# Performance work log

Hardware: AMD Instinct MI355X
Metric: run time of the kernel (lower is better)

The kernel has to match this reference:

```python
import jax, jax.numpy as jnp
import numpy as np

EMBED_DIM = 1024
NUM_HEADS = 16
HEAD_DIM = EMBED_DIM // NUM_HEADS
BATCH = 2
SEQ = 2048


def setup_inputs() -> dict:
    key = jax.random.key(0)
    k_x, k_wi, k_bi, k_wo, k_bo = jax.random.split(key, 5)
    scale_in = 1.0 / np.sqrt(EMBED_DIM)
    x = jax.random.normal(k_x, (BATCH, SEQ, EMBED_DIM), dtype=jnp.float32)
    # nn.Linear stores weight [out, in]; we keep [in, out] for x @ W.
    w_in = jax.random.uniform(k_wi, (EMBED_DIM, 3 * EMBED_DIM), jnp.float32, -scale_in, scale_in)
    b_in = jax.random.uniform(k_bi, (3 * EMBED_DIM,), jnp.float32, -scale_in, scale_in)
    w_out = jax.random.uniform(k_wo, (EMBED_DIM, EMBED_DIM), jnp.float32, -scale_in, scale_in)
    b_out = jax.random.uniform(k_bo, (EMBED_DIM,), jnp.float32, -scale_in, scale_in)
    return {"x": x, "w_in": w_in, "b_in": b_in, "w_out": w_out, "b_out": b_out}


def reference(x, w_in, b_in, w_out, b_out):
    B, S, E = x.shape
    H, D = NUM_HEADS, HEAD_DIM
    inp = x @ w_in + b_in                       # [B,S,3E]
    que, key, val = jnp.split(inp, 3, axis=-1)  # each [B,S,E]
    que = que.reshape(B, S, H, D)
    key = key.reshape(B, S, H, D)
    val = val.reshape(B, S, H, D)
    scores = jnp.einsum('bshd,brhd->bhsr', que, key) * (1.0 / np.sqrt(D))
    weights = jax.nn.softmax(scores, axis=-1)   # [B,H,S,S]
    attn = jnp.einsum('bhsr,brhd->bshd', weights, val).reshape(B, S, E)
    return attn @ w_out + b_out
```

## Files before the change

### kernel.cpp

```cpp
#include <hip/hip_runtime.h>


typedef __bf16 bf16x8 __attribute__((ext_vector_type(8)));
typedef float  f32x4  __attribute__((ext_vector_type(4)));
typedef short  s16x4  __attribute__((ext_vector_type(4)));
typedef short  s16x8  __attribute__((ext_vector_type(8)));

__device__ __forceinline__ unsigned short f2b(float f) {
  unsigned u = __float_as_uint(f);
  unsigned r = u + 0x7fffu + ((u >> 16) & 1u);
  return (unsigned short)(r >> 16);
}

__device__ __forceinline__ unsigned cvt_pk_bf16(float a, float b) {
#if defined(__HIP_DEVICE_COMPILE__)
  unsigned r;
  asm("v_cvt_pk_bf16_f32 %0, %1, %2" : "=v"(r) : "v"(a), "v"(b));
  return r;
#else
  return (unsigned)f2b(a) | ((unsigned)f2b(b) << 16);
#endif
}

__device__ __forceinline__ void gl_lds16(const void* g, void* l) {
  __builtin_amdgcn_global_load_lds(
      (__attribute__((address_space(1))) void*)g,
      (__attribute__((address_space(3))) void*)l, 16, 0, 0);
}

__device__ __forceinline__ f32x4 mfma16x16x16(s16x4 a, s16x4 b, f32x4 c) {
#if defined(__HIP_DEVICE_COMPILE__)
#if __has_builtin(__builtin_amdgcn_mfma_f32_16x16x16bf16_1k)
  return __builtin_amdgcn_mfma_f32_16x16x16bf16_1k(a, b, c, 0, 0, 0);
#else
  s16x8 a8 = {a[0], a[1], a[2], a[3], 0, 0, 0, 0};
  s16x8 b8 = {b[0], b[1], b[2], b[3], 0, 0, 0, 0};
  union U { s16x8 s; bf16x8 v; };
  U ua, ub; ua.s = a8; ub.s = b8;
  return __builtin_amdgcn_mfma_f32_16x16x32_bf16(ua.v, ub.v, c, 0, 0, 0);
#endif
#else
  (void)a; (void)b;
  return c;
#endif
}

__device__ __forceinline__ void transpose_cast_body(
    const float* __restrict__ in, unsigned short* __restrict__ out,
    int R, int C, int bx, int by, int tid, float tile[64][65]) {
  int r0 = by * 64, c0 = bx * 64;
#pragma unroll
  for (int p = 0; p < 16; p++) {
    int i = tid + p * 256;
    int ri = i >> 6, ci = i & 63;
    tile[ri][ci] = in[(size_t)(r0 + ri) * C + c0 + ci];
  }
  __syncthreads();
#pragma unroll
  for (int p = 0; p < 16; p++) {
    int i = tid + p * 256;
    int ci = i >> 6, ri = i & 63;
    out[(size_t)(c0 + ci) * R + r0 + ri] = f2b(tile[ri][ci]);
  }
}

__global__ __launch_bounds__(256) void prep_kernel(
    const float* __restrict__ x, unsigned short* __restrict__ xb,
    const float* __restrict__ w_in, unsigned short* __restrict__ wint,
    const float* __restrict__ w_out, unsigned short* __restrict__ woutt) {
  __shared__ float tile[64][65];
  int bid = blockIdx.x, tid = threadIdx.x;
  if (bid < 4096) {
    int i = bid * 256 + tid;
    float4 v = ((const float4*)x)[i];
    ushort4 o;
    o.x = f2b(v.x); o.y = f2b(v.y); o.z = f2b(v.z); o.w = f2b(v.w);
    ((ushort4*)xb)[i] = o;
  } else if (bid < 4864) {
    int l = bid - 4096;
    transpose_cast_body(w_in, wint, 1024, 3072, l % 48, l / 48, tid, tile);
  } else {
    int l = bid - 4864;
    transpose_cast_body(w_out, woutt, 1024, 1024, l % 16, l / 16, tid, tile);
  }
}

__global__ __launch_bounds__(256) void vt_transpose_kernel(
    const unsigned short* __restrict__ qkv, unsigned short* __restrict__ vt) {
  __shared__ unsigned short tile[64][65];
  int bid = blockIdx.x;
  int st = bid & 31, h = (bid >> 5) & 15, b = bid >> 9;
  int s0 = st * 64;
  int tid = threadIdx.x;
  const unsigned short* src = qkv + (size_t)(b * 2048 + s0) * 3072 + 2048 + h * 64;
#pragma unroll
  for (int p = 0; p < 16; p++) {
    int i = tid + p * 256;
    int sr = i >> 6, d = i & 63;
    tile[sr][d] = src[(size_t)sr * 3072 + d];
  }
  __syncthreads();
  unsigned short* dst = vt + (size_t)(b * 16 + h) * 64 * 2048 + s0;
#pragma unroll
  for (int p = 0; p < 16; p++) {
    int i = tid + p * 256;
    int dr = i >> 6, sc = i & 63;
    dst[(size_t)dr * 2048 + sc] = tile[sc][dr];
  }
}

__global__ __launch_bounds__(256) void gemm_bt1(
    const unsigned short* __restrict__ A, const unsigned short* __restrict__ Bt,
    const float* __restrict__ bias, unsigned short* __restrict__ Cp,
    int M, int N, int K, int qcols, float qscale) {
  __shared__ __align__(16) unsigned short As[128 * 32];
  __shared__ __align__(16) unsigned short Bs[128 * 32];
  int tid = threadIdx.x;
  int wave = tid >> 6, lane = tid & 63;
  int m_l = lane & 15, quad = lane >> 4;
  int wm = (wave >> 1) * 64, wn = (wave & 1) * 64;
  int row = tid >> 2, kp = (tid & 3) << 3;
  const unsigned short* ag = A + (size_t)(blockIdx.y * 128 + row) * K + kp;
  const unsigned short* bg = Bt + (size_t)(blockIdx.x * 128 + row) * K + kp;
  unsigned short* asw = As + wave * 512;
  unsigned short* bsw = Bs + wave * 512;
  f32x4 acc[4][4] = {};
  for (int k0 = 0; k0 < K; k0 += 32) {
    __syncthreads();
    gl_lds16(ag + k0, asw);
    gl_lds16(ag + (size_t)64 * K + k0, asw + 2048);
    gl_lds16(bg + k0, bsw);
    gl_lds16(bg + (size_t)64 * K + k0, bsw + 2048);
    __syncthreads();
    bf16x8 af[4], bf[4];
#pragma unroll
    for (int i = 0; i < 4; i++)
      af[i] = *(const bf16x8*)&As[(wm + i * 16 + m_l) * 32 + quad * 8];
#pragma unroll
    for (int j = 0; j < 4; j++)
      bf[j] = *(const bf16x8*)&Bs[(wn + j * 16 + m_l) * 32 + quad * 8];
#pragma unroll
    for (int i = 0; i < 4; i++)
#pragma unroll
      for (int j = 0; j < 4; j++)
        acc[i][j] = __builtin_amdgcn_mfma_f32_16x16x32_bf16(af[i], bf[j], acc[i][j], 0, 0, 0);
  }
  float bv[4];
#pragma unroll
  for (int j = 0; j < 4; j++) bv[j] = bias[blockIdx.x * 128 + wn + j * 16 + m_l];
#pragma unroll
  for (int i = 0; i < 4; i++) {
    int m = blockIdx.y * 128 + wm + i * 16 + quad * 4;
#pragma unroll
    for (int j = 0; j < 4; j++) {
      int n = blockIdx.x * 128 + wn + j * 16 + m_l;
      float sc = (n < qcols) ? qscale : 1.0f;
#pragma unroll
      for (int r = 0; r < 4; r++) {
        float v = (acc[i][j][r] + bv[j]) * sc;
        Cp[(size_t)(m + r) * N + n] = f2b(v);
      }
    }
  }
}

__global__ __launch_bounds__(256) void gemm_bt2(
    const unsigned short* __restrict__ A, const unsigned short* __restrict__ Bt,
    const float* __restrict__ bias, float* __restrict__ Cp, int M, int N, int K) {
  __shared__ __align__(16) unsigned short As[128 * 32];
  __shared__ __align__(16) unsigned short Bs[64 * 32];
  int tid = threadIdx.x;
  int wave = tid >> 6, lane = tid & 63;
  int m_l = lane & 15, quad = lane >> 4;
  int wm = (wave >> 1) * 64, wn = (wave & 1) * 32;
  int row = tid >> 2, kp = (tid & 3) << 3;
  const unsigned short* ag = A + (size_t)(blockIdx.y * 128 + row) * K + kp;
  const unsigned short* bg = Bt + (size_t)(blockIdx.x * 64 + row) * K + kp;
  unsigned short* asw = As + wave * 512;
  unsigned short* bsw = Bs + wave * 512;
  f32x4 acc[4][2] = {};
  for (int k0 = 0; k0 < K; k0 += 32) {
    __syncthreads();
    gl_lds16(ag + k0, asw);
    gl_lds16(ag + (size_t)64 * K + k0, asw + 2048);
    gl_lds16(bg + k0, bsw);
    __syncthreads();
    bf16x8 af[4], bf[2];
#pragma unroll
    for (int i = 0; i < 4; i++)
      af[i] = *(const bf16x8*)&As[(wm + i * 16 + m_l) * 32 + quad * 8];
#pragma unroll
    for (int j = 0; j < 2; j++)
      bf[j] = *(const bf16x8*)&Bs[(wn + j * 16 + m_l) * 32 + quad * 8];
#pragma unroll
    for (int i = 0; i < 4; i++)
#pragma unroll
      for (int j = 0; j < 2; j++)
        acc[i][j] = __builtin_amdgcn_mfma_f32_16x16x32_bf16(af[i], bf[j], acc[i][j], 0, 0, 0);
  }
  float bv[2];
#pragma unroll
  for (int j = 0; j < 2; j++) bv[j] = bias[blockIdx.x * 64 + wn + j * 16 + m_l];
#pragma unroll
  for (int i = 0; i < 4; i++) {
    int m = blockIdx.y * 128 + wm + i * 16 + quad * 4;
#pragma unroll
    for (int j = 0; j < 2; j++) {
      int n = blockIdx.x * 64 + wn + j * 16 + m_l;
#pragma unroll
      for (int r = 0; r < 4; r++)
        Cp[(size_t)(m + r) * N + n] = acc[i][j][r] + bv[j];
    }
  }
}

__global__ __launch_bounds__(512) void attn_kernel(
    const unsigned short* __restrict__ qkv, const unsigned short* __restrict__ vt,
    unsigned short* __restrict__ aout) {
  __shared__ __align__(16) unsigned short Qs[128 * 64];
  __shared__ __align__(16) unsigned short Ks[64 * 64];
  __shared__ __align__(16) unsigned short Vts[64 * 64];
  int bid = blockIdx.x;
  int qt = bid & 15, h = (bid >> 4) & 15, b = bid >> 8;
  int tid = threadIdx.x, wave = tid >> 6;
  int lane = tid & 63;
  int m_l = lane & 15, quad = lane >> 4;
  int q0 = qt * 128;
  const unsigned short* qb = qkv + (size_t)b * 2048 * 3072 + h * 64;
  const unsigned short* kb = qb + 1024;
  const unsigned short* vtb = vt + (size_t)(b * 16 + h) * 64 * 2048;

  int srow = tid >> 3;
  int sd0 = ((tid & 7) ^ (srow & 7)) * 8;

  gl_lds16(qb + (size_t)(q0 + srow) * 3072 + sd0, Qs + wave * 512);
  gl_lds16(qb + (size_t)(q0 + 64 + srow) * 3072 + sd0, Qs + 4096 + wave * 512);
  __syncthreads();

  int ml7 = m_l & 7;
  int sw0 = ((quad ^ ml7) * 8);
  int sw1 = (((quad + 4) ^ ml7) * 8);

  int qrow = (wave * 16 + m_l) * 64;
  bf16x8 qf0 = *(const bf16x8*)&Qs[qrow + sw0];
  bf16x8 qf1 = *(const bf16x8*)&Qs[qrow + sw1];

  int kbase = m_l * 64;
  int vbase = m_l * 64 + (quad & 1) * 4;
  int qh = quad >> 1;

  const s16x4 ones = {0x3F80, 0x3F80, 0x3F80, 0x3F80};

  f32x4 o[4] = {};
  f32x4 lacc = {};

  for (int kt = 0; kt < 2048; kt += 64) {
    __syncthreads();
    gl_lds16(kb + (size_t)(kt + srow) * 3072 + sd0, Ks + wave * 512);
    gl_lds16(vtb + (size_t)srow * 2048 + kt + sd0, Vts + wave * 512);
    __syncthreads();

#pragma unroll
    for (int t = 0; t < 4; t++) {
      bf16x8 kf0 = *(const bf16x8*)&Ks[kbase + t * 1024 + sw0];
      bf16x8 kf1 = *(const bf16x8*)&Ks[kbase + t * 1024 + sw1];
      f32x4 z = {};
      f32x4 s = __builtin_amdgcn_mfma_f32_16x16x32_bf16(kf0, qf0, z, 0, 0, 0);
      s = __builtin_amdgcn_mfma_f32_16x16x32_bf16(kf1, qf1, s, 0, 0, 0);
      union { uint2 u; s16x4 s4; } pk;
      pk.u.x = cvt_pk_bf16(__builtin_exp2f(s[0]), __builtin_exp2f(s[1]));
      pk.u.y = cvt_pk_bf16(__builtin_exp2f(s[2]), __builtin_exp2f(s[3]));
      lacc = mfma16x16x16(ones, pk.s4, lacc);
      int voff = vbase + (((t * 2 + qh) ^ ml7) * 8);
#pragma unroll
      for (int dt = 0; dt < 4; dt++) {
        s16x4 vf = *(const s16x4*)&Vts[voff + dt * 1024];
        o[dt] = mfma16x16x16(vf, pk.s4, o[dt]);
      }
    }
  }

  float rl = 1.0f / lacc[0];

  unsigned short* ob = aout + (size_t)(b * 2048 + q0 + wave * 16 + m_l) * 1024 +
                       h * 64 + quad * 4;
#pragma unroll
  for (int dt = 0; dt < 4; dt++) {
    union { uint2 u; ushort4 w; } pk;
    pk.u.x = cvt_pk_bf16(o[dt][0] * rl, o[dt][1] * rl);
    pk.u.y = cvt_pk_bf16(o[dt][2] * rl, o[dt][3] * rl);
    *(ushort4*)&ob[dt * 16] = pk.w;
  }
}

extern "C" void kernel_launch(void* const* d_in, const int* in_sizes, int n_in,
                              void* d_out, int out_size, void* d_ws, size_t ws_size,
                              hipStream_t stream) {
  (void)in_sizes; (void)n_in; (void)out_size; (void)ws_size;
  const float* x     = (const float*)d_in[0];
  const float* w_in  = (const float*)d_in[1];
  const float* b_in  = (const float*)d_in[2];
  const float* w_out = (const float*)d_in[3];
  const float* b_out = (const float*)d_in[4];
  char* ws = (char*)d_ws;
  unsigned short* xb    = (unsigned short*)(ws + 0);
  unsigned short* wint  = (unsigned short*)(ws + 8388608);
  unsigned short* woutt = (unsigned short*)(ws + 14680064);
  unsigned short* qkv   = (unsigned short*)(ws + 16777216);
  unsigned short* vt    = (unsigned short*)(ws + 41943040);
  unsigned short* attn  = (unsigned short*)(ws + 50331648);
  float* out = (float*)d_out;

  const float QSCALE = 0.125f * 1.44269504088896f;

  prep_kernel<<<5120, 256, 0, stream>>>(x, xb, w_in, wint, w_out, woutt);
  gemm_bt1<<<dim3(24, 32), 256, 0, stream>>>(xb, wint, b_in, qkv, 4096, 3072, 1024,
                                             1024, QSCALE);
  vt_transpose_kernel<<<1024, 256, 0, stream>>>(qkv, vt);
  attn_kernel<<<512, 512, 0, stream>>>(qkv, vt, attn);
  gemm_bt2<<<dim3(16, 32), 256, 0, stream>>>(attn, woutt, b_out, out, 4096, 1024, 1024);
}
```

Before: 207.6 us.

## Rewrite attention inner loop with 32x32x16 MFMA and permlane32 swaps

The attention kernel moves from 16x16 MFMA tiles with 8 waves per block to 32x32x16 MFMA tiles with 4 waves per block, each wave covering 32 query rows. The row sum is now accumulated on VALU from the exponentials instead of with an extra MFMA against a ones vector. The P fragments for the PV product are re-laid out in registers with v_permlane32_swap. The aim is fewer MFMA instructions, fewer LDS fragment reads per FLOP, and no redundant sum-MFMA, at the cost of more registers per wave and fewer waves per block.

```diff
diff --git a/kernel.cpp b/kernel.cpp
--- a/kernel.cpp
+++ b/kernel.cpp
@@ -3,6 +3,7 @@
 
 typedef __bf16 bf16x8 __attribute__((ext_vector_type(8)));
 typedef float  f32x4  __attribute__((ext_vector_type(4)));
+typedef float  f32x16 __attribute__((ext_vector_type(16)));
 typedef short  s16x4  __attribute__((ext_vector_type(4)));
 typedef short  s16x8  __attribute__((ext_vector_type(8)));
 
@@ -22,27 +23,16 @@
 #endif
 }
 
+__device__ __forceinline__ void permlane32_swap(unsigned& a, unsigned& b) {
+#if defined(__HIP_DEVICE_COMPILE__)
+  asm("v_permlane32_swap_b32 %0, %1" : "+v"(a), "+v"(b));
+#endif
+}
+
 __device__ __forceinline__ void gl_lds16(const void* g, void* l) {
   __builtin_amdgcn_global_load_lds(
       (__attribute__((address_space(1))) void*)g,
       (__attribute__((address_space(3))) void*)l, 16, 0, 0);
-}
-
-__device__ __forceinline__ f32x4 mfma16x16x16(s16x4 a, s16x4 b, f32x4 c) {
-#if defined(__HIP_DEVICE_COMPILE__)
-#if __has_builtin(__builtin_amdgcn_mfma_f32_16x16x16bf16_1k)
-  return __builtin_amdgcn_mfma_f32_16x16x16bf16_1k(a, b, c, 0, 0, 0);
-#else
-  s16x8 a8 = {a[0], a[1], a[2], a[3], 0, 0, 0, 0};
-  s16x8 b8 = {b[0], b[1], b[2], b[3], 0, 0, 0, 0};
-  union U { s16x8 s; bf16x8 v; };
-  U ua, ub; ua.s = a8; ub.s = b8;
-  return __builtin_amdgcn_mfma_f32_16x16x32_bf16(ua.v, ub.v, c, 0, 0, 0);
-#endif
-#else
-  (void)a; (void)b;
-  return c;
-#endif
 }
 
 __device__ __forceinline__ void transpose_cast_body(
@@ -214,7 +204,7 @@
   }
 }
 
-__global__ __launch_bounds__(512) void attn_kernel(
+__global__ __launch_bounds__(256) void attn_kernel(
     const unsigned short* __restrict__ qkv, const unsigned short* __restrict__ vt,
     unsigned short* __restrict__ aout) {
   __shared__ __align__(16) unsigned short Qs[128 * 64];
@@ -222,9 +212,8 @@
   __shared__ __align__(16) unsigned short Vts[64 * 64];
   int bid = blockIdx.x;
   int qt = bid & 15, h = (bid >> 4) & 15, b = bid >> 8;
-  int tid = threadIdx.x, wave = tid >> 6;
-  int lane = tid & 63;
-  int m_l = lane & 15, quad = lane >> 4;
+  int tid = threadIdx.x, wave = tid >> 6, lane = tid & 63;
+  int l31 = lane & 31, hi = lane >> 5, l7 = lane & 7;
   int q0 = qt * 128;
   const unsigned short* qb = qkv + (size_t)b * 2048 * 3072 + h * 64;
   const unsigned short* kb = qb + 1024;
@@ -233,64 +222,76 @@
   int srow = tid >> 3;
   int sd0 = ((tid & 7) ^ (srow & 7)) * 8;
 
-  gl_lds16(qb + (size_t)(q0 + srow) * 3072 + sd0, Qs + wave * 512);
-  gl_lds16(qb + (size_t)(q0 + 64 + srow) * 3072 + sd0, Qs + 4096 + wave * 512);
+#pragma unroll
+  for (int p = 0; p < 4; p++)
+    gl_lds16(qb + (size_t)(q0 + p * 32 + srow) * 3072 + sd0, Qs + p * 2048 + wave * 512);
   __syncthreads();
 
-  int ml7 = m_l & 7;
-  int sw0 = ((quad ^ ml7) * 8);
-  int sw1 = (((quad + 4) ^ ml7) * 8);
-
-  int qrow = (wave * 16 + m_l) * 64;
-  bf16x8 qf0 = *(const bf16x8*)&Qs[qrow + sw0];
-  bf16x8 qf1 = *(const bf16x8*)&Qs[qrow + sw1];
-
-  int kbase = m_l * 64;
-  int vbase = m_l * 64 + (quad & 1) * 4;
-  int qh = quad >> 1;
-
-  const s16x4 ones = {0x3F80, 0x3F80, 0x3F80, 0x3F80};
-
-  f32x4 o[4] = {};
-  f32x4 lacc = {};
+  bf16x8 qf[4];
+  int qrow = (wave * 32 + l31) * 64;
+#pragma unroll
+  for (int ks = 0; ks < 4; ks++)
+    qf[ks] = *(const bf16x8*)&Qs[qrow + ((2 * ks + hi) ^ l7) * 8];
+
+  f32x16 oacc[2] = {};
+  float lsum = 0.0f;
 
   for (int kt = 0; kt < 2048; kt += 64) {
     __syncthreads();
-    gl_lds16(kb + (size_t)(kt + srow) * 3072 + sd0, Ks + wave * 512);
-    gl_lds16(vtb + (size_t)srow * 2048 + kt + sd0, Vts + wave * 512);
-    __syncthreads();
-
-#pragma unroll
-    for (int t = 0; t < 4; t++) {
-      bf16x8 kf0 = *(const bf16x8*)&Ks[kbase + t * 1024 + sw0];
-      bf16x8 kf1 = *(const bf16x8*)&Ks[kbase + t * 1024 + sw1];
-      f32x4 z = {};
-      f32x4 s = __builtin_amdgcn_mfma_f32_16x16x32_bf16(kf0, qf0, z, 0, 0, 0);
-      s = __builtin_amdgcn_mfma_f32_16x16x32_bf16(kf1, qf1, s, 0, 0, 0);
-      union { uint2 u; s16x4 s4; } pk;
-      pk.u.x = cvt_pk_bf16(__builtin_exp2f(s[0]), __builtin_exp2f(s[1]));
-      pk.u.y = cvt_pk_bf16(__builtin_exp2f(s[2]), __builtin_exp2f(s[3]));
-      lacc = mfma16x16x16(ones, pk.s4, lacc);
-      int voff = vbase + (((t * 2 + qh) ^ ml7) * 8);
-#pragma unroll
-      for (int dt = 0; dt < 4; dt++) {
-        s16x4 vf = *(const s16x4*)&Vts[voff + dt * 1024];
-        o[dt] = mfma16x16x16(vf, pk.s4, o[dt]);
+#pragma unroll
+    for (int p = 0; p < 2; p++) {
+      gl_lds16(kb + (size_t)(kt + p * 32 + srow) * 3072 + sd0, Ks + p * 2048 + wave * 512);
+      gl_lds16(vtb + (size_t)(p * 32 + srow) * 2048 + kt + sd0, Vts + p * 2048 + wave * 512);
+    }
+    __syncthreads();
+
+#pragma unroll
+    for (int tt = 0; tt < 2; tt++) {
+      f32x16 sacc = {};
+#pragma unroll
+      for (int ks = 0; ks < 4; ks++) {
+        bf16x8 kf = *(const bf16x8*)&Ks[(tt * 32 + l31) * 64 + ((2 * ks + hi) ^ l7) * 8];
+        sacc = __builtin_amdgcn_mfma_f32_32x32x16_bf16(kf, qf[ks], sacc, 0, 0, 0);
       }
-    }
-  }
-
-  float rl = 1.0f / lacc[0];
-
-  unsigned short* ob = aout + (size_t)(b * 2048 + q0 + wave * 16 + m_l) * 1024 +
-                       h * 64 + quad * 4;
-#pragma unroll
-  for (int dt = 0; dt < 4; dt++) {
-    union { uint2 u; ushort4 w; } pk;
-    pk.u.x = cvt_pk_bf16(o[dt][0] * rl, o[dt][1] * rl);
-    pk.u.y = cvt_pk_bf16(o[dt][2] * rl, o[dt][3] * rl);
-    *(ushort4*)&ob[dt * 16] = pk.w;
-  }
+      float pv[16];
+#pragma unroll
+      for (int i = 0; i < 16; i++) {
+        pv[i] = __builtin_exp2f(sacc[i]);
+        lsum += pv[i];
+      }
+#pragma unroll
+      for (int g = 0; g < 2; g++) {
+        unsigned a0 = cvt_pk_bf16(pv[8 * g + 0], pv[8 * g + 1]);
+        unsigned a1 = cvt_pk_bf16(pv[8 * g + 2], pv[8 * g + 3]);
+        unsigned b0 = cvt_pk_bf16(pv[8 * g + 4], pv[8 * g + 5]);
+        unsigned b1 = cvt_pk_bf16(pv[8 * g + 6], pv[8 * g + 7]);
+        permlane32_swap(a0, b0);
+        permlane32_swap(a1, b1);
+        union { unsigned u[4]; bf16x8 v; } pf;
+        pf.u[0] = a0; pf.u[1] = a1; pf.u[2] = b0; pf.u[3] = b1;
+        int kc = tt * 2 + g;
+#pragma unroll
+        for (int dt = 0; dt < 2; dt++) {
+          bf16x8 vf = *(const bf16x8*)&Vts[(dt * 32 + l31) * 64 + ((kc * 2 + hi) ^ l7) * 8];
+          oacc[dt] = __builtin_amdgcn_mfma_f32_32x32x16_bf16(vf, pf.v, oacc[dt], 0, 0, 0);
+        }
+      }
+    }
+  }
+
+  float lp = lsum + __shfl_xor(lsum, 32, 64);
+  float rl = 1.0f / lp;
+
+  unsigned short* ob = aout + (size_t)(b * 2048 + q0 + wave * 32 + l31) * 1024 + h * 64;
+#pragma unroll
+  for (int dt = 0; dt < 2; dt++)
+#pragma unroll
+    for (int rq = 0; rq < 4; rq++) {
+      union { uint2 u; ushort4 w; } pk;
+      pk.u.x = cvt_pk_bf16(oacc[dt][4 * rq + 0] * rl, oacc[dt][4 * rq + 1] * rl);
+      pk.u.y = cvt_pk_bf16(oacc[dt][4 * rq + 2] * rl, oacc[dt][4 * rq + 3] * rl);
+      *(ushort4*)&ob[dt * 32 + rq * 8 + hi * 4] = pk.w;
+    }
 }
 
 extern "C" void kernel_launch(void* const* d_in, const int* in_sizes, int n_in,
@@ -317,6 +318,6 @@
   gemm_bt1<<<dim3(24, 32), 256, 0, stream>>>(xb, wint, b_in, qkv, 4096, 3072, 1024,
                                              1024, QSCALE);
   vt_transpose_kernel<<<1024, 256, 0, stream>>>(qkv, vt);
-  attn_kernel<<<512, 512, 0, stream>>>(qkv, vt, attn);
+  attn_kernel<<<512, 256, 0, stream>>>(qkv, vt, attn);
   gemm_bt2<<<dim3(16, 32), 256, 0, stream>>>(attn, woutt, b_out, out, 4096, 1024, 1024);
 }
```

New measurement: 212.8 us. 1.03x slower.
